# Kernel tuning notes

Hardware: AMD Instinct MI355X
Metric: run time of the kernel (lower is better)

The kernel has to match this reference:

```python
import jax, jax.numpy as jnp
import numpy as np

QMAX = 127.0  # 2**(bits-1) - 1 for bits=8, signed symmetric


def _quantize_signed_symmetric(t):
    # per-tensor symmetric: scale = max|t| / qmax, q = clamp(round(t/scale))
    scale = jnp.max(jnp.abs(t)) / QMAX
    q = jnp.clip(jnp.round(t / scale), -QMAX, QMAX)
    return q, scale


def setup_inputs() -> dict:
    key = jax.random.key(0)
    k1, k2, k3 = jax.random.split(key, 3)
    N, D_IN, D_OUT = 16384, 1024, 1024
    x = jax.random.normal(k1, (N, D_IN), dtype=jnp.float32)
    weight = jax.random.normal(k2, (D_OUT, D_IN), dtype=jnp.float32) * 0.02
    bias = jax.random.normal(k3, (D_OUT,), dtype=jnp.float32) * 0.01
    return {"x": x, "weight": weight, "bias": bias}


def reference(x, weight, bias):
    # weight quantization (cached in torch; recomputed here, same math)
    qw, w_scale = _quantize_signed_symmetric(weight)
    qw_t = qw.astype(jnp.int32).T            # [D_IN, D_OUT]
    # activation quantization
    qx, x_scale = _quantize_signed_symmetric(x)
    qx = qx.astype(jnp.int32)                # [N, D_IN]
    # int32 matmul, then per-tensor dequant + bias
    acc = qx @ qw_t                          # int32 [N, D_OUT]
    y = acc.astype(jnp.float32) * (x_scale * w_scale)
    return y + bias
```

## Files before the change

### kernel.cpp

```cpp
#include <hip/hip_runtime.h>

#define QMAX 127.0f

typedef int int4v __attribute__((ext_vector_type(4)));
typedef float float4v __attribute__((ext_vector_type(4)));

__device__ __forceinline__ float amax4(float4 v) {
    return fmaxf(fmaxf(fabsf(v.x), fabsf(v.y)), fmaxf(fabsf(v.z), fabsf(v.w)));
}

__global__ void absmax2_kernel(const float4* __restrict__ px, int n4x,
                               const float4* __restrict__ pw, int n4w,
                               int gx, int* __restrict__ amax) {
    const float4* p; int n4; int* out; int nb, bid;
    if ((int)blockIdx.x < gx) { p = px; n4 = n4x; out = amax + 0; nb = gx; bid = blockIdx.x; }
    else { p = pw; n4 = n4w; out = amax + 1; nb = gridDim.x - gx; bid = blockIdx.x - gx; }
    const int S = nb * blockDim.x;
    int i = bid * blockDim.x + threadIdx.x;
    float a = 0.f, b = 0.f, c = 0.f, d = 0.f;
    for (; i + 3 * S < n4; i += 4 * S) {
        float4 v0 = p[i];
        float4 v1 = p[i + S];
        float4 v2 = p[i + 2 * S];
        float4 v3 = p[i + 3 * S];
        a = fmaxf(a, amax4(v0));
        b = fmaxf(b, amax4(v1));
        c = fmaxf(c, amax4(v2));
        d = fmaxf(d, amax4(v3));
    }
    for (; i < n4; i += S) a = fmaxf(a, amax4(p[i]));
    float m = fmaxf(fmaxf(a, b), fmaxf(c, d));
    for (int off = 32; off; off >>= 1) m = fmaxf(m, __shfl_down(m, off, 64));
    __shared__ float sm[4];
    if ((threadIdx.x & 63) == 0) sm[threadIdx.x >> 6] = m;
    __syncthreads();
    if (threadIdx.x == 0) {
        float bm = fmaxf(fmaxf(sm[0], sm[1]), fmaxf(sm[2], sm[3]));
        atomicMax(out, (int)__float_as_uint(bm));
    }
}

__device__ __forceinline__ int qone(float v, float s) {
    float q = fminf(fmaxf(rintf(v / s), -QMAX), QMAX);
    return (int)q;
}
__device__ __forceinline__ int qpack4(float4 v, float s) {
    return (qone(v.x, s) & 255) | ((qone(v.y, s) & 255) << 8) |
           ((qone(v.z, s) & 255) << 16) | ((qone(v.w, s) & 255) << 24);
}

__global__ void quantw_kernel(const float4* __restrict__ sw, int4v* __restrict__ dw,
                              int n16w, int kshift, int KC,
                              const int* __restrict__ amax) {
    const float scale = __uint_as_float((unsigned)amax[1]) / QMAX;
    const int stride = gridDim.x * blockDim.x;
    for (int i = blockIdx.x * blockDim.x + threadIdx.x; i < n16w; i += stride) {
        float4 v0 = sw[4 * i + 0];
        float4 v1 = sw[4 * i + 1];
        float4 v2 = sw[4 * i + 2];
        float4 v3 = sw[4 * i + 3];
        int4v o = { qpack4(v0, scale), qpack4(v1, scale),
                    qpack4(v2, scale), qpack4(v3, scale) };
        const int n = i >> kshift;
        const int kg = i & ((1 << kshift) - 1);
        const int kc = kg >> 2, q = kg & 3;
        const int g = n >> 4, r = n & 15;
        dw[(g * KC + kc) * 64 + q * 16 + r] = o;
    }
}

__global__ __launch_bounds__(1024, 4) void gemm_i8_kernel(
        const float* __restrict__ x, const char* __restrict__ qb,
        const float4* __restrict__ bias4, const int* __restrict__ amax,
        float* __restrict__ out, int M, int N, int K) {
    extern __shared__ char sA[];

    const int KC = K >> 6;
    const int tid = threadIdx.x;
    const int lane = tid & 63;
    const int w = tid >> 6;
    const int m0 = blockIdx.x * 64;

    const char* bbase = qb + (size_t)(w * 4) * KC * 1024 + lane * 16;

#define LOADB(Bb, kc)                                                        \
    do { _Pragma("unroll") for (int j = 0; j < 4; ++j)                       \
        Bb[j] = *(const int4v*)(bbase + ((size_t)j * KC + (kc)) * 1024);     \
    } while (0)
#define LOADA(Af, kc)                                                        \
    do { _Pragma("unroll") for (int i = 0; i < 4; ++i)                       \
        Af[i] = sAv[i * K + (kc) * 64 + lane];                               \
    } while (0)
#define MF(Bb, Af)                                                           \
    do { _Pragma("unroll") for (int j = 0; j < 4; ++j)                       \
        _Pragma("unroll") for (int i = 0; i < 4; ++i)                        \
            acc[j][i] = __builtin_amdgcn_mfma_i32_16x16x64_i8(               \
                Bb[j], Af[i], acc[j][i], 0, 0, 0);                           \
    } while (0)

    int4v B0[4], B1[4], Af[4];
    LOADB(B0, 0);

    const float xs = __uint_as_float((unsigned)amax[0]) / QMAX;
    int4v* sAv_w = (int4v*)sA;
    const int kcs = __builtin_ctz(KC);
    const int PPW = KC >> 2;
#pragma unroll 2
    for (int p = 0; p < PPW; ++p) {
        const int pair = w * PPW + p;
        const int i = pair >> kcs;
        const int kc = pair & (KC - 1);
        const int row = m0 + i * 16 + (lane & 15);
        const int k0 = kc * 64 + (lane >> 4) * 16;
        const float4* src = (const float4*)(x + (size_t)row * K + k0);
        float4 v0 = src[0];
        float4 v1 = src[1];
        float4 v2 = src[2];
        float4 v3 = src[3];
        int4v o = { qpack4(v0, xs), qpack4(v1, xs),
                    qpack4(v2, xs), qpack4(v3, xs) };
        sAv_w[i * K + kc * 64 + lane] = o;
    }
    __syncthreads();

    int4v acc[4][4];
    const int4v zero = {0, 0, 0, 0};
#pragma unroll
    for (int j = 0; j < 4; ++j)
#pragma unroll
        for (int i = 0; i < 4; ++i) acc[j][i] = zero;

    const int4v* sAv = (const int4v*)sA;

#pragma unroll 1
    for (int kc = 0; kc + 2 < KC; kc += 2) {
        LOADB(B1, kc + 1);
        LOADA(Af, kc);
        MF(B0, Af);
        LOADB(B0, kc + 2);
        LOADA(Af, kc + 1);
        MF(B1, Af);
    }
    LOADB(B1, KC - 1);
    LOADA(Af, KC - 2);
    MF(B0, Af);
    LOADA(Af, KC - 1);
    MF(B1, Af);

    const float sc = (__uint_as_float((unsigned)amax[0]) / QMAX) *
                     (__uint_as_float((unsigned)amax[1]) / QMAX);
    const int quad = lane >> 4;
    const int rbase = m0 + (lane & 15);
    const int cb4 = w * 16;
#pragma unroll
    for (int j = 0; j < 4; ++j) {
        const float4 bv = bias4[cb4 + j * 4 + quad];
#pragma unroll
        for (int i = 0; i < 4; ++i) {
            const int row = rbase + i * 16;
            float4v v;
            v[0] = (float)acc[j][i][0] * sc + bv.x;
            v[1] = (float)acc[j][i][1] * sc + bv.y;
            v[2] = (float)acc[j][i][2] * sc + bv.z;
            v[3] = (float)acc[j][i][3] * sc + bv.w;
            *((float4v*)(out + (size_t)row * N) + cb4 + j * 4 + quad) = v;
        }
    }
}

extern "C" void kernel_launch(void* const* d_in, const int* in_sizes, int n_in,
                              void* d_out, int out_size, void* d_ws, size_t ws_size,
                              hipStream_t stream) {
    const float* x = (const float*)d_in[0];
    const float* w = (const float*)d_in[1];
    const float* bias = (const float*)d_in[2];
    float* out = (float*)d_out;

    const int xn = in_sizes[0];
    const int wn = in_sizes[1];
    const int N = in_sizes[2];
    const int K = wn / N;
    const int M = xn / K;
    const int KC = K >> 6;
    const int kshift = __builtin_ctz(K >> 4);

    int* amax = (int*)d_ws;
    char* qw = (char*)d_ws + 1024;

    const int GAX = 2048, GAW = 256;
    absmax2_kernel<<<GAX + GAW, 256, 0, stream>>>(
        (const float4*)x, xn / 4, (const float4*)w, wn / 4, GAX, amax);

    quantw_kernel<<<256, 256, 0, stream>>>(
        (const float4*)w, (int4v*)qw, wn / 16, kshift, KC, amax);

    gemm_i8_kernel<<<M / 64, 1024, 64 * K, stream>>>(
        x, qw, (const float4*)bias, amax, out, M, N, K);
}
```

Baseline: 161.4 us.

## Fuse absmax, weight quantization and int8 GEMM into one cooperative kernel

Replaces the three-kernel sequence (absmax reduction, weight quantization, GEMM) with a single cooperative kernel that uses two grid-wide syncs: each block reduces the absmax of its own x rows plus a slice of the weight, quantizes a slice of the weight and its own A tile into shared memory, then runs the MFMA k-loop. The aim is to remove kernel launch gaps and the separate read of x for the reduction, since each block re-reads the rows it just reduced. This needs all 256 blocks of 1024 threads with 64 KB LDS resident at once and falls back to the old path if the cooperative launch fails. Grid syncs add their own latency. The amax buffer is never zeroed, but the old code had the same pattern.

```diff
diff --git a/kernel.cpp b/kernel.cpp
--- a/kernel.cpp
+++ b/kernel.cpp
@@ -1,4 +1,7 @@
 #include <hip/hip_runtime.h>
+#include <hip/hip_cooperative_groups.h>
+
+namespace cg = cooperative_groups;
 
 #define QMAX 127.0f
 
@@ -7,6 +10,192 @@
 
 __device__ __forceinline__ float amax4(float4 v) {
     return fmaxf(fmaxf(fabsf(v.x), fabsf(v.y)), fmaxf(fabsf(v.z), fabsf(v.w)));
+}
+__device__ __forceinline__ int qone(float v, float s) {
+    float q = fminf(fmaxf(rintf(v / s), -QMAX), QMAX);
+    return (int)q;
+}
+__device__ __forceinline__ int qpack4(float4 v, float s) {
+    return (qone(v.x, s) & 255) | ((qone(v.y, s) & 255) << 8) |
+           ((qone(v.z, s) & 255) << 16) | ((qone(v.w, s) & 255) << 24);
+}
+
+#define LOADB(Bb, kc)                                                        \
+    do { _Pragma("unroll") for (int j = 0; j < 4; ++j)                       \
+        Bb[j] = *(const int4v*)(bbase + ((size_t)j * KC + (kc)) * 1024);     \
+    } while (0)
+#define LOADA(Af, kc)                                                        \
+    do { _Pragma("unroll") for (int i = 0; i < 4; ++i)                       \
+        Af[i] = sAv[i * K + (kc) * 64 + lane];                               \
+    } while (0)
+#define MF(Bb, Af)                                                           \
+    do { _Pragma("unroll") for (int j = 0; j < 4; ++j)                       \
+        _Pragma("unroll") for (int i = 0; i < 4; ++i)                        \
+            acc[j][i] = __builtin_amdgcn_mfma_i32_16x16x64_i8(               \
+                Bb[j], Af[i], acc[j][i], 0, 0, 0);                           \
+    } while (0)
+
+__device__ __forceinline__ void quant_w_slice(const float* __restrict__ w,
+                                              int4v* __restrict__ qw, int i,
+                                              int kshift, int KC, float wsc) {
+    const float4* sw = (const float4*)w;
+    float4 v0 = sw[4 * i + 0];
+    float4 v1 = sw[4 * i + 1];
+    float4 v2 = sw[4 * i + 2];
+    float4 v3 = sw[4 * i + 3];
+    int4v o = { qpack4(v0, wsc), qpack4(v1, wsc),
+                qpack4(v2, wsc), qpack4(v3, wsc) };
+    const int n = i >> kshift;
+    const int kg = i & ((1 << kshift) - 1);
+    const int kc = kg >> 2, q = kg & 3;
+    const int g = n >> 4, r = n & 15;
+    qw[(g * KC + kc) * 64 + q * 16 + r] = o;
+}
+
+__device__ __forceinline__ void stage_quant_A(const float* __restrict__ x,
+                                              char* sA, int m0, int K, int KC,
+                                              int lane, int wv, float xs) {
+    int4v* sw4 = (int4v*)sA;
+    const int kcs = __builtin_ctz(KC);
+    const int PPW = KC >> 2;
+#pragma unroll 2
+    for (int pp = 0; pp < PPW; ++pp) {
+        const int pair = wv * PPW + pp;
+        const int i = pair >> kcs;
+        const int kc = pair & (KC - 1);
+        const int row = m0 + i * 16 + (lane & 15);
+        const int k0 = kc * 64 + (lane >> 4) * 16;
+        const float4* src = (const float4*)(x + (size_t)row * K + k0);
+        float4 v0 = src[0];
+        float4 v1 = src[1];
+        float4 v2 = src[2];
+        float4 v3 = src[3];
+        int4v o = { qpack4(v0, xs), qpack4(v1, xs),
+                    qpack4(v2, xs), qpack4(v3, xs) };
+        sw4[i * K + kc * 64 + lane] = o;
+    }
+}
+
+__device__ __forceinline__ void kloop_epilogue(const char* sAc,
+                                               const char* __restrict__ qb,
+                                               const float4* __restrict__ bias4,
+                                               float* __restrict__ out,
+                                               int N, int K, int KC,
+                                               int lane, int wv, int m0, float sc) {
+    const int4v* sAv = (const int4v*)sAc;
+    const char* bbase = qb + (size_t)(wv * 4) * KC * 1024 + lane * 16;
+
+    int4v acc[4][4];
+    const int4v zero = {0, 0, 0, 0};
+#pragma unroll
+    for (int j = 0; j < 4; ++j)
+#pragma unroll
+        for (int i = 0; i < 4; ++i) acc[j][i] = zero;
+
+    int4v B0[4], B1[4], Af[4];
+    LOADB(B0, 0);
+#pragma unroll 1
+    for (int kc = 0; kc + 2 < KC; kc += 2) {
+        LOADB(B1, kc + 1);
+        LOADA(Af, kc);
+        MF(B0, Af);
+        LOADB(B0, kc + 2);
+        LOADA(Af, kc + 1);
+        MF(B1, Af);
+    }
+    LOADB(B1, KC - 1);
+    LOADA(Af, KC - 2);
+    MF(B0, Af);
+    LOADA(Af, KC - 1);
+    MF(B1, Af);
+
+    const int quad = lane >> 4;
+    const int rbase = m0 + (lane & 15);
+    const int cb4 = wv * 16;
+#pragma unroll
+    for (int j = 0; j < 4; ++j) {
+        const float4 bv = bias4[cb4 + j * 4 + quad];
+#pragma unroll
+        for (int i = 0; i < 4; ++i) {
+            const int row = rbase + i * 16;
+            float4v v;
+            v[0] = (float)acc[j][i][0] * sc + bv.x;
+            v[1] = (float)acc[j][i][1] * sc + bv.y;
+            v[2] = (float)acc[j][i][2] * sc + bv.z;
+            v[3] = (float)acc[j][i][3] * sc + bv.w;
+            *((float4v*)(out + (size_t)row * N) + cb4 + j * 4 + quad) = v;
+        }
+    }
+}
+
+__global__ __launch_bounds__(1024, 4) void fused_ql_kernel(
+        const float* __restrict__ x, const float* __restrict__ w,
+        const float4* __restrict__ bias4, float* __restrict__ out,
+        int* __restrict__ amax, int4v* __restrict__ qw,
+        int M, int N, int K) {
+    extern __shared__ char sA[];
+
+    const int KC = K >> 6;
+    const int tid = threadIdx.x;
+    const int lane = tid & 63;
+    const int wv = tid >> 6;
+    const int bid = blockIdx.x;
+    const int m0 = bid * 64;
+
+    {
+        const float4* xp = (const float4*)(x + (size_t)m0 * K);
+        const int n4s = K << 4;
+        float a0 = 0.f, a1 = 0.f, a2 = 0.f, a3 = 0.f;
+        for (int i = tid; i < n4s; i += 4096) {
+            a0 = fmaxf(a0, amax4(xp[i]));
+            a1 = fmaxf(a1, amax4(xp[i + 1024]));
+            a2 = fmaxf(a2, amax4(xp[i + 2048]));
+            a3 = fmaxf(a3, amax4(xp[i + 3072]));
+        }
+        float ax = fmaxf(fmaxf(a0, a1), fmaxf(a2, a3));
+        float aw = 0.f;
+        const float4* wp = (const float4*)w;
+        const int n4w = (N * K) >> 2;
+        const int gs = (int)gridDim.x << 10;
+        for (int i = (bid << 10) + tid; i < n4w; i += gs)
+            aw = fmaxf(aw, amax4(wp[i]));
+        for (int off = 32; off; off >>= 1) {
+            ax = fmaxf(ax, __shfl_down(ax, off, 64));
+            aw = fmaxf(aw, __shfl_down(aw, off, 64));
+        }
+        float* red = (float*)sA;
+        if (lane == 0) { red[wv] = ax; red[16 + wv] = aw; }
+        __syncthreads();
+        if (tid == 0) {
+            float mx = red[0], mw = red[16];
+            for (int k2 = 1; k2 < 16; ++k2) {
+                mx = fmaxf(mx, red[k2]);
+                mw = fmaxf(mw, red[16 + k2]);
+            }
+            atomicMax(amax + 0, (int)__float_as_uint(mx));
+            atomicMax(amax + 1, (int)__float_as_uint(mw));
+        }
+    }
+    cg::this_grid().sync();
+
+    const float xs = __uint_as_float((unsigned)__hip_atomic_load(
+                         amax + 0, __ATOMIC_RELAXED, __HIP_MEMORY_SCOPE_AGENT)) / QMAX;
+    const float wsc = __uint_as_float((unsigned)__hip_atomic_load(
+                         amax + 1, __ATOMIC_RELAXED, __HIP_MEMORY_SCOPE_AGENT)) / QMAX;
+
+    {
+        const int n16w = (N * K) >> 4;
+        const int per = n16w / (int)gridDim.x;
+        const int kshift = __builtin_ctz(K >> 4);
+        for (int t = tid; t < per; t += 1024)
+            quant_w_slice(w, qw, bid * per + t, kshift, KC, wsc);
+    }
+    stage_quant_A(x, sA, m0, K, KC, lane, wv, xs);
+
+    cg::this_grid().sync();
+
+    kloop_epilogue(sA, (const char*)qw, bias4, out, N, K, KC, lane, wv, m0,
+                   xs * wsc);
 }
 
 __global__ void absmax2_kernel(const float4* __restrict__ px, int n4x,
@@ -40,132 +229,30 @@
     }
 }
 
-__device__ __forceinline__ int qone(float v, float s) {
-    float q = fminf(fmaxf(rintf(v / s), -QMAX), QMAX);
-    return (int)q;
-}
-__device__ __forceinline__ int qpack4(float4 v, float s) {
-    return (qone(v.x, s) & 255) | ((qone(v.y, s) & 255) << 8) |
-           ((qone(v.z, s) & 255) << 16) | ((qone(v.w, s) & 255) << 24);
-}
-
-__global__ void quantw_kernel(const float4* __restrict__ sw, int4v* __restrict__ dw,
+__global__ void quantw_kernel(const float* __restrict__ w, int4v* __restrict__ dw,
                               int n16w, int kshift, int KC,
                               const int* __restrict__ amax) {
     const float scale = __uint_as_float((unsigned)amax[1]) / QMAX;
     const int stride = gridDim.x * blockDim.x;
-    for (int i = blockIdx.x * blockDim.x + threadIdx.x; i < n16w; i += stride) {
-        float4 v0 = sw[4 * i + 0];
-        float4 v1 = sw[4 * i + 1];
-        float4 v2 = sw[4 * i + 2];
-        float4 v3 = sw[4 * i + 3];
-        int4v o = { qpack4(v0, scale), qpack4(v1, scale),
-                    qpack4(v2, scale), qpack4(v3, scale) };
-        const int n = i >> kshift;
-        const int kg = i & ((1 << kshift) - 1);
-        const int kc = kg >> 2, q = kg & 3;
-        const int g = n >> 4, r = n & 15;
-        dw[(g * KC + kc) * 64 + q * 16 + r] = o;
-    }
-}
-
-__global__ __launch_bounds__(1024, 4) void gemm_i8_kernel(
+    for (int i = blockIdx.x * blockDim.x + threadIdx.x; i < n16w; i += stride)
+        quant_w_slice(w, dw, i, kshift, KC, scale);
+}
+
+__global__ __launch_bounds__(1024, 4) void gemm_fused_kernel(
         const float* __restrict__ x, const char* __restrict__ qb,
         const float4* __restrict__ bias4, const int* __restrict__ amax,
         float* __restrict__ out, int M, int N, int K) {
     extern __shared__ char sA[];
-
     const int KC = K >> 6;
     const int tid = threadIdx.x;
     const int lane = tid & 63;
-    const int w = tid >> 6;
+    const int wv = tid >> 6;
     const int m0 = blockIdx.x * 64;
-
-    const char* bbase = qb + (size_t)(w * 4) * KC * 1024 + lane * 16;
-
-#define LOADB(Bb, kc)                                                        \
-    do { _Pragma("unroll") for (int j = 0; j < 4; ++j)                       \
-        Bb[j] = *(const int4v*)(bbase + ((size_t)j * KC + (kc)) * 1024);     \
-    } while (0)
-#define LOADA(Af, kc)                                                        \
-    do { _Pragma("unroll") for (int i = 0; i < 4; ++i)                       \
-        Af[i] = sAv[i * K + (kc) * 64 + lane];                               \
-    } while (0)
-#define MF(Bb, Af)                                                           \
-    do { _Pragma("unroll") for (int j = 0; j < 4; ++j)                       \
-        _Pragma("unroll") for (int i = 0; i < 4; ++i)                        \
-            acc[j][i] = __builtin_amdgcn_mfma_i32_16x16x64_i8(               \
-                Bb[j], Af[i], acc[j][i], 0, 0, 0);                           \
-    } while (0)
-
-    int4v B0[4], B1[4], Af[4];
-    LOADB(B0, 0);
-
     const float xs = __uint_as_float((unsigned)amax[0]) / QMAX;
-    int4v* sAv_w = (int4v*)sA;
-    const int kcs = __builtin_ctz(KC);
-    const int PPW = KC >> 2;
-#pragma unroll 2
-    for (int p = 0; p < PPW; ++p) {
-        const int pair = w * PPW + p;
-        const int i = pair >> kcs;
-        const int kc = pair & (KC - 1);
-        const int row = m0 + i * 16 + (lane & 15);
-        const int k0 = kc * 64 + (lane >> 4) * 16;
-        const float4* src = (const float4*)(x + (size_t)row * K + k0);
-        float4 v0 = src[0];
-        float4 v1 = src[1];
-        float4 v2 = src[2];
-        float4 v3 = src[3];
-        int4v o = { qpack4(v0, xs), qpack4(v1, xs),
-                    qpack4(v2, xs), qpack4(v3, xs) };
-        sAv_w[i * K + kc * 64 + lane] = o;
-    }
+    const float wsc = __uint_as_float((unsigned)amax[1]) / QMAX;
+    stage_quant_A(x, sA, m0, K, KC, lane, wv, xs);
     __syncthreads();
-
-    int4v acc[4][4];
-    const int4v zero = {0, 0, 0, 0};
-#pragma unroll
-    for (int j = 0; j < 4; ++j)
-#pragma unroll
-        for (int i = 0; i < 4; ++i) acc[j][i] = zero;
-
-    const int4v* sAv = (const int4v*)sA;
-
-#pragma unroll 1
-    for (int kc = 0; kc + 2 < KC; kc += 2) {
-        LOADB(B1, kc + 1);
-        LOADA(Af, kc);
-        MF(B0, Af);
-        LOADB(B0, kc + 2);
-        LOADA(Af, kc + 1);
-        MF(B1, Af);
-    }
-    LOADB(B1, KC - 1);
-    LOADA(Af, KC - 2);
-    MF(B0, Af);
-    LOADA(Af, KC - 1);
-    MF(B1, Af);
-
-    const float sc = (__uint_as_float((unsigned)amax[0]) / QMAX) *
-                     (__uint_as_float((unsigned)amax[1]) / QMAX);
-    const int quad = lane >> 4;
-    const int rbase = m0 + (lane & 15);
-    const int cb4 = w * 16;
-#pragma unroll
-    for (int j = 0; j < 4; ++j) {
-        const float4 bv = bias4[cb4 + j * 4 + quad];
-#pragma unroll
-        for (int i = 0; i < 4; ++i) {
-            const int row = rbase + i * 16;
-            float4v v;
-            v[0] = (float)acc[j][i][0] * sc + bv.x;
-            v[1] = (float)acc[j][i][1] * sc + bv.y;
-            v[2] = (float)acc[j][i][2] * sc + bv.z;
-            v[3] = (float)acc[j][i][3] * sc + bv.w;
-            *((float4v*)(out + (size_t)row * N) + cb4 + j * 4 + quad) = v;
-        }
-    }
+    kloop_epilogue(sA, qb, bias4, out, N, K, KC, lane, wv, m0, xs * wsc);
 }
 
 extern "C" void kernel_launch(void* const* d_in, const int* in_sizes, int n_in,
@@ -185,15 +272,24 @@
     const int kshift = __builtin_ctz(K >> 4);
 
     int* amax = (int*)d_ws;
-    char* qw = (char*)d_ws + 1024;
-
-    const int GAX = 2048, GAW = 256;
-    absmax2_kernel<<<GAX + GAW, 256, 0, stream>>>(
-        (const float4*)x, xn / 4, (const float4*)w, wn / 4, GAX, amax);
-
-    quantw_kernel<<<256, 256, 0, stream>>>(
-        (const float4*)w, (int4v*)qw, wn / 16, kshift, KC, amax);
-
-    gemm_i8_kernel<<<M / 64, 1024, 64 * K, stream>>>(
-        x, qw, (const float4*)bias, amax, out, M, N, K);
-}
+    char* qwb = (char*)d_ws + 1024;
+    int4v* qwv = (int4v*)qwb;
+    const float4* bias4 = (const float4*)bias;
+
+    const int grid = M / 64;
+    void* args[] = { (void*)&x, (void*)&w, (void*)&bias4, (void*)&out,
+                     (void*)&amax, (void*)&qwv,
+                     (void*)&M, (void*)&N, (void*)&K };
+    hipError_t err = hipLaunchCooperativeKernel(
+        (const void*)fused_ql_kernel, dim3(grid), dim3(1024), args,
+        (unsigned)(64 * K), stream);
+    if (err != hipSuccess) {
+        const int GAX = 2048, GAW = 256;
+        absmax2_kernel<<<GAX + GAW, 256, 0, stream>>>(
+            (const float4*)x, xn / 4, (const float4*)w, wn / 4, GAX, amax);
+        quantw_kernel<<<256, 256, 0, stream>>>(
+            w, qwv, wn / 16, kshift, KC, amax);
+        gemm_fused_kernel<<<M / 64, 1024, 64 * K, stream>>>(
+            x, qwb, bias4, amax, out, M, N, K);
+    }
+}
```

Result: slower. 219.0 us (+35.7%).

## Stream activation quantization into double-buffered LDS chunks overlapped with MFMA loop

Applied to the files above, without the earlier changes.

Instead of quantizing the block's entire 64xK activation tile into shared memory before any compute, the kernel now processes K in 256-wide chunks. Each wave prefetches the next chunk's fp32 x values into registers, quantizes them, and writes them into an alternate 16KB LDS buffer while MFMAs run on the current chunk. The aim is to hide x load latency behind compute and cut LDS from 64KB to 32KB per block, which may allow more resident blocks. In exchange it adds a __syncthreads per chunk and holds extra prefetch registers.

```diff
diff --git a/kernel.cpp b/kernel.cpp
--- a/kernel.cpp
+++ b/kernel.cpp
@@ -7,6 +7,14 @@
 
 __device__ __forceinline__ float amax4(float4 v) {
     return fmaxf(fmaxf(fabsf(v.x), fabsf(v.y)), fmaxf(fabsf(v.z), fabsf(v.w)));
+}
+__device__ __forceinline__ int qone(float v, float s) {
+    float q = fminf(fmaxf(rintf(v / s), -QMAX), QMAX);
+    return (int)q;
+}
+__device__ __forceinline__ int qpack4(float4 v, float s) {
+    return (qone(v.x, s) & 255) | ((qone(v.y, s) & 255) << 8) |
+           ((qone(v.z, s) & 255) << 16) | ((qone(v.w, s) & 255) << 24);
 }
 
 __global__ void absmax2_kernel(const float4* __restrict__ px, int n4x,
@@ -40,15 +48,6 @@
     }
 }
 
-__device__ __forceinline__ int qone(float v, float s) {
-    float q = fminf(fmaxf(rintf(v / s), -QMAX), QMAX);
-    return (int)q;
-}
-__device__ __forceinline__ int qpack4(float4 v, float s) {
-    return (qone(v.x, s) & 255) | ((qone(v.y, s) & 255) << 8) |
-           ((qone(v.z, s) & 255) << 16) | ((qone(v.w, s) & 255) << 24);
-}
-
 __global__ void quantw_kernel(const float4* __restrict__ sw, int4v* __restrict__ dw,
                               int n16w, int kshift, int KC,
                               const int* __restrict__ amax) {
@@ -76,20 +75,30 @@
     extern __shared__ char sA[];
 
     const int KC = K >> 6;
+    const int CH = KC >> 2;
     const int tid = threadIdx.x;
     const int lane = tid & 63;
-    const int w = tid >> 6;
+    const int wv = tid >> 6;
     const int m0 = blockIdx.x * 64;
 
-    const char* bbase = qb + (size_t)(w * 4) * KC * 1024 + lane * 16;
+    const int si = wv >> 2;
+    const int skcl = wv & 3;
+    const int srow = m0 + si * 16 + (lane & 15);
+    const int sk0 = skcl * 64 + (lane >> 4) * 16;
+    const float* sbase = x + (size_t)srow * K + sk0;
+    const int sslot = si * 256 + skcl * 64 + lane;
+
+    const float xs = __uint_as_float((unsigned)amax[0]) / QMAX;
+
+    const char* bbase = qb + (size_t)(wv * 4) * KC * 1024 + lane * 16;
 
 #define LOADB(Bb, kc)                                                        \
     do { _Pragma("unroll") for (int j = 0; j < 4; ++j)                       \
         Bb[j] = *(const int4v*)(bbase + ((size_t)j * KC + (kc)) * 1024);     \
     } while (0)
-#define LOADA(Af, kc)                                                        \
+#define LOADA(Af, kcl)                                                       \
     do { _Pragma("unroll") for (int i = 0; i < 4; ++i)                       \
-        Af[i] = sAv[i * K + (kc) * 64 + lane];                               \
+        Af[i] = sAv[i * 256 + (kcl) * 64 + lane];                            \
     } while (0)
 #define MF(Bb, Af)                                                           \
     do { _Pragma("unroll") for (int j = 0; j < 4; ++j)                       \
@@ -97,30 +106,22 @@
             acc[j][i] = __builtin_amdgcn_mfma_i32_16x16x64_i8(               \
                 Bb[j], Af[i], acc[j][i], 0, 0, 0);                           \
     } while (0)
+#define ISSUEX(h)                                                            \
+    do { const float4* sp = (const float4*)(sbase + (h) * 256);              \
+        xr0 = sp[0]; xr1 = sp[1]; xr2 = sp[2]; xr3 = sp[3];                  \
+    } while (0)
+#define QWRITE(h)                                                            \
+    do { int4v o = { qpack4(xr0, xs), qpack4(xr1, xs),                       \
+                     qpack4(xr2, xs), qpack4(xr3, xs) };                     \
+        ((int4v*)(sA + ((h) & 1) * 16384))[sslot] = o;                       \
+    } while (0)
 
+    float4 xr0, xr1, xr2, xr3;
     int4v B0[4], B1[4], Af[4];
+
+    ISSUEX(0);
     LOADB(B0, 0);
-
-    const float xs = __uint_as_float((unsigned)amax[0]) / QMAX;
-    int4v* sAv_w = (int4v*)sA;
-    const int kcs = __builtin_ctz(KC);
-    const int PPW = KC >> 2;
-#pragma unroll 2
-    for (int p = 0; p < PPW; ++p) {
-        const int pair = w * PPW + p;
-        const int i = pair >> kcs;
-        const int kc = pair & (KC - 1);
-        const int row = m0 + i * 16 + (lane & 15);
-        const int k0 = kc * 64 + (lane >> 4) * 16;
-        const float4* src = (const float4*)(x + (size_t)row * K + k0);
-        float4 v0 = src[0];
-        float4 v1 = src[1];
-        float4 v2 = src[2];
-        float4 v3 = src[3];
-        int4v o = { qpack4(v0, xs), qpack4(v1, xs),
-                    qpack4(v2, xs), qpack4(v3, xs) };
-        sAv_w[i * K + kc * 64 + lane] = o;
-    }
+    QWRITE(0);
     __syncthreads();
 
     int4v acc[4][4];
@@ -130,28 +131,27 @@
 #pragma unroll
         for (int i = 0; i < 4; ++i) acc[j][i] = zero;
 
-    const int4v* sAv = (const int4v*)sA;
+#pragma unroll 1
+    for (int h = 0; h < CH; ++h) {
+        const int4v* sAv = (const int4v*)(sA + (h & 1) * 16384);
+        const int kc0 = h * 4;
+        const bool more = (h + 1 < CH);
+        if (more) ISSUEX(h + 1);
+        LOADB(B1, kc0 + 1); LOADA(Af, 0); MF(B0, Af);
+        LOADB(B0, kc0 + 2); LOADA(Af, 1); MF(B1, Af);
+        LOADB(B1, kc0 + 3); LOADA(Af, 2); MF(B0, Af);
+        if (more) LOADB(B0, kc0 + 4);
+        LOADA(Af, 3); MF(B1, Af);
+        if (more) {
+            QWRITE(h + 1);
+            __syncthreads();
+        }
+    }
 
-#pragma unroll 1
-    for (int kc = 0; kc + 2 < KC; kc += 2) {
-        LOADB(B1, kc + 1);
-        LOADA(Af, kc);
-        MF(B0, Af);
-        LOADB(B0, kc + 2);
-        LOADA(Af, kc + 1);
-        MF(B1, Af);
-    }
-    LOADB(B1, KC - 1);
-    LOADA(Af, KC - 2);
-    MF(B0, Af);
-    LOADA(Af, KC - 1);
-    MF(B1, Af);
-
-    const float sc = (__uint_as_float((unsigned)amax[0]) / QMAX) *
-                     (__uint_as_float((unsigned)amax[1]) / QMAX);
+    const float sc = xs * (__uint_as_float((unsigned)amax[1]) / QMAX);
     const int quad = lane >> 4;
     const int rbase = m0 + (lane & 15);
-    const int cb4 = w * 16;
+    const int cb4 = wv * 16;
 #pragma unroll
     for (int j = 0; j < 4; ++j) {
         const float4 bv = bias4[cb4 + j * 4 + quad];
@@ -194,6 +194,6 @@
     quantw_kernel<<<256, 256, 0, stream>>>(
         (const float4*)w, (int4v*)qw, wn / 16, kshift, KC, amax);
 
-    gemm_i8_kernel<<<M / 64, 1024, 64 * K, stream>>>(
+    gemm_i8_kernel<<<M / 64, 1024, 32768, stream>>>(
         x, qw, (const float4*)bias, amax, out, M, N, K);
 }
```

After: 191.2 us. 1.18x slower.
